# Kernel tuning notes

Hardware: AMD Instinct MI355X
Metric: run time of the kernel (lower is better)

The kernel has to match this reference:

```python
import jax, jax.numpy as jnp
import numpy as np

B, S, D, H = 2, 2048, 2048, 16
DK = D // H
THETA = 10000.0


def setup_inputs() -> dict:
    key = jax.random.key(0)
    ks = jax.random.split(key, 5)
    scale = 0.02
    return {
        "x": jax.random.normal(ks[0], (B, S, D), dtype=jnp.float32),
        "W_Q": jax.random.normal(ks[1], (D, D), dtype=jnp.float32) * scale,
        "W_K": jax.random.normal(ks[2], (D, D), dtype=jnp.float32) * scale,
        "W_V": jax.random.normal(ks[3], (D, D), dtype=jnp.float32) * scale,
        "W_O": jax.random.normal(ks[4], (D, D), dtype=jnp.float32) * scale,
        "token_positions": jnp.arange(S, dtype=jnp.int32),
    }


def _rope(x, pos):
    # x: [B, S, H, DK]; pos: [S]. Interleaved-pair rotation (cs336 RoPE).
    half = DK // 2
    inv_freq = THETA ** (-(jnp.arange(half, dtype=jnp.float32) / half))  # [half]
    ang = pos.astype(jnp.float32)[:, None] * inv_freq[None, :]           # [S, half]
    cos = jnp.cos(ang)[None, :, None, :]                                 # [1,S,1,half]
    sin = jnp.sin(ang)[None, :, None, :]
    x1, x2 = x[..., ::2], x[..., 1::2]
    r1 = x1 * cos - x2 * sin
    r2 = x1 * sin + x2 * cos
    return jnp.stack([r1, r2], axis=-1).reshape(x.shape)


def reference(x, W_Q, W_K, W_V, W_O, token_positions):
    # QKV projections (Linear with no bias: y = x @ W^T)
    Q = (x @ W_Q.T).reshape(B, S, H, DK)
    K = (x @ W_K.T).reshape(B, S, H, DK)
    V = (x @ W_V.T).reshape(B, S, H, DK)
    Q = _rope(Q, token_positions)
    K = _rope(K, token_positions)
    scores = jnp.einsum("bqhd,bkhd->bhqk", Q, K) / jnp.sqrt(jnp.float32(DK))
    causal = jnp.tril(jnp.ones((S, S), dtype=bool))  # True = attend
    scores = jnp.where(causal[None, None], scores, -jnp.inf)
    attn = jax.nn.softmax(scores, axis=-1)
    out = jnp.einsum("bhqk,bkhd->bqhd", attn, V).reshape(B, S, D)
    return out @ W_O.T
```

## Files before the change

### kernel.cpp

```cpp
#include <hip/hip_runtime.h>
#include <hip/hip_bf16.h>
#include <cstdint>
#include <cstddef>

#define B_ 2
#define S_ 2048
#define D_ 2048
#define H_ 16
#define DK_ 128
#define M_ (B_*S_)

typedef __attribute__((ext_vector_type(8))) __bf16 bf16x8;
typedef __attribute__((ext_vector_type(4))) float f32x4;
typedef __attribute__((ext_vector_type(16))) float f32x16;

__device__ __forceinline__ unsigned short f2bf(float f) {
  union { float f; unsigned int u; } v; v.f = f;
  unsigned int r = (v.u + 0x7fffu + ((v.u >> 16) & 1u)) >> 16;
  return (unsigned short)r;
}
__device__ __forceinline__ float bf2f(unsigned short b) {
  union { unsigned int u; float f; } v; v.u = ((unsigned int)b) << 16;
  return v.f;
}

__device__ __forceinline__ void gld16(const void* g, void* l) {
  __builtin_amdgcn_global_load_lds(
      (const __attribute__((address_space(1))) unsigned int*)g,
      (__attribute__((address_space(3))) unsigned int*)l, 16, 0, 0);
}

__global__ void cvt_all(const float* __restrict__ x,  const float* __restrict__ Wq,
                        const float* __restrict__ Wk, const float* __restrict__ Wv,
                        const float* __restrict__ Wo, unsigned short* __restrict__ dst) {
  size_t i = ((size_t)blockIdx.x * blockDim.x + threadIdx.x) * 4;
  const float* src;
  size_t off;
  if (i < ((size_t)M_ * D_)) {
    src = x; off = i;
  } else {
    size_t j = i - (size_t)M_ * D_;
    int w = (int)(j >> 22);
    off = j & ((1u << 22) - 1);
    src = (w == 0) ? Wq : (w == 1) ? Wk : (w == 2) ? Wv : Wo;
  }
  float4 v = *(const float4*)(src + off);
  dst[i+0] = f2bf(v.x); dst[i+1] = f2bf(v.y);
  dst[i+2] = f2bf(v.z); dst[i+3] = f2bf(v.w);
}

__global__ __launch_bounds__(512, 2) void gemm_qkv(const unsigned short* __restrict__ A,
                                                   const unsigned short* __restrict__ W0,
                                                   const unsigned short* __restrict__ W1,
                                                   const unsigned short* __restrict__ W2,
                                                   unsigned short* __restrict__ C0,
                                                   unsigned short* __restrict__ C1,
                                                   unsigned short* __restrict__ C2,
                                                   int M, int N, int K) {
  __shared__ unsigned short sA[2][2][256 * 32];
  __shared__ unsigned short sB[2][2][256 * 32];
  const int id   = blockIdx.x;
  const int tid  = threadIdx.x;
  const int lane = tid & 63;
  const int wid  = tid >> 6;
  const int l16 = lane & 15, quad = lane >> 4;
  const int col16 = quad ^ ((lane >> 1) & 3);
  const int qk_log = (lane & 3) ^ ((lane >> 3) & 3);
  const int srow = lane >> 2;
  const int NT = K >> 6;

  if (id < 256) {
    const int z = id >> 7, r = id & 127;
    const unsigned short* Bt = z ? W1 : W0;
    unsigned short* Cout = z ? C1 : C0;
    const int bm = (r >> 3) * 256, bn = (r & 7) * 256;
    const int wm = wid >> 2, wn = wid & 3;

    f32x4 acc[8][4];
    #pragma unroll
    for (int i = 0; i < 8; ++i)
      #pragma unroll
      for (int j = 0; j < 4; ++j)
        acc[i][j] = (f32x4){0.f, 0.f, 0.f, 0.f};

    auto stage = [&](const unsigned short* __restrict__ g, int rowbase,
                     unsigned short* l, int t, int kh) {
      const unsigned short* src = g + (size_t)rowbase * K + t * 64 + kh * 32 + qk_log * 8;
      #pragma unroll
      for (int p = 0; p < 2; ++p) {
        const int i = wid * 2 + p;
        gld16(src + (size_t)(i * 16 + srow) * K, l + i * 512);
      }
    };

    stage(A,  bm, &sA[0][0][0], 0, 0);
    stage(Bt, bn, &sB[0][0][0], 0, 0);
    stage(A,  bm, &sA[0][1][0], 0, 1);
    stage(Bt, bn, &sB[0][1][0], 0, 1);
    stage(A,  bm, &sA[1][0][0], 1, 0);
    stage(Bt, bn, &sB[1][0][0], 1, 0);
    asm volatile("s_waitcnt vmcnt(4)" ::: "memory");
    __builtin_amdgcn_s_barrier();

    for (int t = 0; t < NT; ++t) {
      const int buf = t & 1;
      bf16x8 bfrag[4];
      #pragma unroll
      for (int ph = 0; ph < 4; ++ph) {
        const int ks = ph >> 1;
        const int mh = ph & 1;
        bf16x8 afrag[4];
        const unsigned short* aP = &sA[buf][ks][0] +
            (size_t)((wm * 128 + mh * 64 + l16) * 4 + col16) * 8;
        #pragma unroll
        for (int mf = 0; mf < 4; ++mf)
          afrag[mf] = *(const bf16x8*)(aP + mf * 512);
        if (mh == 0) {
          const unsigned short* bP = &sB[buf][ks][0] +
              (size_t)((wn * 64 + l16) * 4 + col16) * 8;
          #pragma unroll
          for (int nf = 0; nf < 4; ++nf)
            bfrag[nf] = *(const bf16x8*)(bP + nf * 512);
        }
        if (ph == 0)      { if (t + 1 < NT) stage(A,  bm, &sA[buf ^ 1][1][0], t + 1, 1); }
        else if (ph == 1) { if (t + 1 < NT) stage(Bt, bn, &sB[buf ^ 1][1][0], t + 1, 1); }
        else if (ph == 2) { if (t + 2 < NT) stage(A,  bm, &sA[buf][0][0],     t + 2, 0); }
        else              { if (t + 2 < NT) stage(Bt, bn, &sB[buf][0][0],     t + 2, 0); }

        __builtin_amdgcn_s_barrier();
        asm volatile("s_waitcnt lgkmcnt(0)" ::: "memory");
        __builtin_amdgcn_s_setprio(1);
        #pragma unroll
        for (int nf = 0; nf < 4; ++nf)
          #pragma unroll
          for (int mf = 0; mf < 4; ++mf)
            acc[mh * 4 + mf][nf] = __builtin_amdgcn_mfma_f32_16x16x32_bf16(
                afrag[mf], bfrag[nf], acc[mh * 4 + mf][nf], 0, 0, 0);
        __builtin_amdgcn_s_setprio(0);
        if (ph == 3) {
          if (t + 2 < NT) asm volatile("s_waitcnt vmcnt(4)" ::: "memory");
          else            asm volatile("s_waitcnt vmcnt(0)" ::: "memory");
        }
        __builtin_amdgcn_s_barrier();
      }
    }

    #pragma unroll
    for (int mf = 0; mf < 8; ++mf) {
      const int row = bm + wm * 128 + mf * 16 + quad * 4;
      #pragma unroll
      for (int nf = 0; nf < 4; ++nf) {
        const int col = bn + wn * 64 + nf * 16 + l16;
        #pragma unroll
        for (int rr = 0; rr < 4; ++rr)
          Cout[(size_t)(row + rr) * N + col] = f2bf(acc[mf][nf][rr]);
      }
    }
  } else {
    const int r = id - 256;
    const unsigned short* Bt = W2;
    unsigned short* Cout = C2;
    const int bm = (r >> 3) * 128, bn = (r & 7) * 256;
    const int wm = wid >> 2, wn = wid & 3;

    f32x4 acc[4][4];
    #pragma unroll
    for (int i = 0; i < 4; ++i)
      #pragma unroll
      for (int j = 0; j < 4; ++j)
        acc[i][j] = (f32x4){0.f, 0.f, 0.f, 0.f};

    auto stageB = [&](unsigned short* l, int t, int kh) {
      const unsigned short* src = Bt + (size_t)bn * K + t * 64 + kh * 32 + qk_log * 8;
      #pragma unroll
      for (int p = 0; p < 2; ++p) {
        const int i = wid * 2 + p;
        gld16(src + (size_t)(i * 16 + srow) * K, l + i * 512);
      }
    };
    auto stageA = [&](unsigned short* l, int t, int kh) {
      const unsigned short* src = A + (size_t)bm * K + t * 64 + kh * 32 + qk_log * 8;
      gld16(src + (size_t)(wid * 16 + srow) * K, l + wid * 512);
    };

    stageA(&sA[0][0][0], 0, 0); stageB(&sB[0][0][0], 0, 0);
    stageA(&sA[0][1][0], 0, 1); stageB(&sB[0][1][0], 0, 1);
    stageA(&sA[1][0][0], 1, 0); stageB(&sB[1][0][0], 1, 0);
    asm volatile("s_waitcnt vmcnt(3)" ::: "memory");
    __builtin_amdgcn_s_barrier();

    for (int t = 0; t < NT; ++t) {
      const int buf = t & 1;
      #pragma unroll
      for (int ph = 0; ph < 2; ++ph) {
        bf16x8 afrag[4], bfrag[4];
        const unsigned short* aP = &sA[buf][ph][0] +
            (size_t)((wm * 64 + l16) * 4 + col16) * 8;
        #pragma unroll
        for (int mf = 0; mf < 4; ++mf)
          afrag[mf] = *(const bf16x8*)(aP + mf * 512);
        const unsigned short* bP = &sB[buf][ph][0] +
            (size_t)((wn * 64 + l16) * 4 + col16) * 8;
        #pragma unroll
        for (int nf = 0; nf < 4; ++nf)
          bfrag[nf] = *(const bf16x8*)(bP + nf * 512);

        if (ph == 0) { if (t + 1 < NT) { stageA(&sA[buf ^ 1][1][0], t + 1, 1);
                                         stageB(&sB[buf ^ 1][1][0], t + 1, 1); } }
        else         { if (t + 2 < NT) { stageA(&sA[buf][0][0], t + 2, 0);
                                         stageB(&sB[buf][0][0], t + 2, 0); } }

        __builtin_amdgcn_s_barrier();
        asm volatile("s_waitcnt lgkmcnt(0)" ::: "memory");
        __builtin_amdgcn_s_setprio(1);
        #pragma unroll
        for (int nf = 0; nf < 4; ++nf)
          #pragma unroll
          for (int mf = 0; mf < 4; ++mf)
            acc[mf][nf] = __builtin_amdgcn_mfma_f32_16x16x32_bf16(
                afrag[mf], bfrag[nf], acc[mf][nf], 0, 0, 0);
        __builtin_amdgcn_s_setprio(0);
        if (ph == 1) {
          if (t + 2 < NT) asm volatile("s_waitcnt vmcnt(3)" ::: "memory");
          else            asm volatile("s_waitcnt vmcnt(0)" ::: "memory");
        }
        __builtin_amdgcn_s_barrier();
      }
    }

    #pragma unroll
    for (int mf = 0; mf < 4; ++mf) {
      const int row = bm + wm * 64 + mf * 16 + quad * 4;
      #pragma unroll
      for (int nf = 0; nf < 4; ++nf) {
        const int col = bn + wn * 64 + nf * 16 + l16;
        #pragma unroll
        for (int rr = 0; rr < 4; ++rr)
          Cout[(size_t)(row + rr) * N + col] = f2bf(acc[mf][nf][rr]);
      }
    }
  }
}

__global__ __launch_bounds__(512, 2) void gemm_out(const unsigned short* __restrict__ A,
                                                   const unsigned short* __restrict__ Bt,
                                                   float* __restrict__ C,
                                                   int M, int N, int K) {
  __shared__ unsigned short sA[2][2][256 * 32];
  __shared__ unsigned short sB[2][2][128 * 32];
  const int id   = blockIdx.x;
  const int tid  = threadIdx.x;
  const int lane = tid & 63;
  const int wid  = tid >> 6;
  const int l16 = lane & 15, quad = lane >> 4;
  const int col16 = quad ^ ((lane >> 1) & 3);
  const int qk_log = (lane & 3) ^ ((lane >> 3) & 3);
  const int srow = lane >> 2;
  const int NT = K >> 6;
  const int bm = (id >> 4) * 256, bn = (id & 15) * 128;
  const int wm = wid >> 1, wn = wid & 1;

  f32x4 acc[4][4];
  #pragma unroll
  for (int i = 0; i < 4; ++i)
    #pragma unroll
    for (int j = 0; j < 4; ++j)
      acc[i][j] = (f32x4){0.f, 0.f, 0.f, 0.f};

  auto stageA = [&](unsigned short* l, int t, int kh) {
    const unsigned short* src = A + (size_t)bm * K + t * 64 + kh * 32 + qk_log * 8;
    #pragma unroll
    for (int p = 0; p < 2; ++p) {
      const int i = wid * 2 + p;
      gld16(src + (size_t)(i * 16 + srow) * K, l + i * 512);
    }
  };
  auto stageB = [&](unsigned short* l, int t, int kh) {
    const unsigned short* src = Bt + (size_t)bn * K + t * 64 + kh * 32 + qk_log * 8;
    gld16(src + (size_t)(wid * 16 + srow) * K, l + wid * 512);
  };

  stageA(&sA[0][0][0], 0, 0); stageB(&sB[0][0][0], 0, 0);
  stageA(&sA[0][1][0], 0, 1); stageB(&sB[0][1][0], 0, 1);
  stageA(&sA[1][0][0], 1, 0); stageB(&sB[1][0][0], 1, 0);
  asm volatile("s_waitcnt vmcnt(3)" ::: "memory");
  __builtin_amdgcn_s_barrier();

  for (int t = 0; t < NT; ++t) {
    const int buf = t & 1;
    #pragma unroll
    for (int ph = 0; ph < 2; ++ph) {
      bf16x8 afrag[4], bfrag[4];
      const unsigned short* aP = &sA[buf][ph][0] +
          (size_t)((wm * 64 + l16) * 4 + col16) * 8;
      #pragma unroll
      for (int mf = 0; mf < 4; ++mf)
        afrag[mf] = *(const bf16x8*)(aP + mf * 512);
      const unsigned short* bP = &sB[buf][ph][0] +
          (size_t)((wn * 64 + l16) * 4 + col16) * 8;
      #pragma unroll
      for (int nf = 0; nf < 4; ++nf)
        bfrag[nf] = *(const bf16x8*)(bP + nf * 512);

      if (ph == 0) { if (t + 1 < NT) { stageA(&sA[buf ^ 1][1][0], t + 1, 1);
                                       stageB(&sB[buf ^ 1][1][0], t + 1, 1); } }
      else         { if (t + 2 < NT) { stageA(&sA[buf][0][0], t + 2, 0);
                                       stageB(&sB[buf][0][0], t + 2, 0); } }

      __builtin_amdgcn_s_barrier();
      asm volatile("s_waitcnt lgkmcnt(0)" ::: "memory");
      __builtin_amdgcn_s_setprio(1);
      #pragma unroll
      for (int nf = 0; nf < 4; ++nf)
        #pragma unroll
        for (int mf = 0; mf < 4; ++mf)
          acc[mf][nf] = __builtin_amdgcn_mfma_f32_16x16x32_bf16(
              afrag[mf], bfrag[nf], acc[mf][nf], 0, 0, 0);
      __builtin_amdgcn_s_setprio(0);
      if (ph == 1) {
        if (t + 2 < NT) asm volatile("s_waitcnt vmcnt(3)" ::: "memory");
        else            asm volatile("s_waitcnt vmcnt(0)" ::: "memory");
      }
      __builtin_amdgcn_s_barrier();
    }
  }

  #pragma unroll
  for (int mf = 0; mf < 4; ++mf) {
    const int row = bm + wm * 64 + mf * 16 + quad * 4;
    #pragma unroll
    for (int nf = 0; nf < 4; ++nf) {
      const int col = bn + wn * 64 + nf * 16 + l16;
      #pragma unroll
      for (int rr = 0; rr < 4; ++rr)
        C[(size_t)(row + rr) * N + col] = acc[mf][nf][rr];
    }
  }
}

__global__ void rope_kernel(unsigned short* __restrict__ Q, unsigned short* __restrict__ K,
                            const int* __restrict__ pos) {
  int idx = blockIdx.x * blockDim.x + threadIdx.x;
  int i = idx & 63;
  int h = (idx >> 6) & (H_ - 1);
  int s = (idx >> 10) & (S_ - 1);
  int b = idx >> 21;
  float p = (float)pos[s];
  float inv = __expf(-(float)i * (9.210340371976184f / 64.0f));
  float ang = p * inv;
  float sn, cs;
  __sincosf(ang, &sn, &cs);
  size_t base = (((size_t)b * S_ + s) * D_) + (size_t)h * DK_ + 2 * i;
  unsigned int q2 = *(const unsigned int*)(Q + base);
  float x1 = bf2f((unsigned short)(q2 & 0xffffu)), x2 = bf2f((unsigned short)(q2 >> 16));
  unsigned int lo = f2bf(x1 * cs - x2 * sn), hi = f2bf(x1 * sn + x2 * cs);
  *(unsigned int*)(Q + base) = lo | (hi << 16);
  unsigned int k2 = *(const unsigned int*)(K + base);
  x1 = bf2f((unsigned short)(k2 & 0xffffu)); x2 = bf2f((unsigned short)(k2 >> 16));
  lo = f2bf(x1 * cs - x2 * sn); hi = f2bf(x1 * sn + x2 * cs);
  *(unsigned int*)(K + base) = lo | (hi << 16);
}

__global__ __launch_bounds__(256) void transpose_bf16(const unsigned short* __restrict__ src,
                                                      unsigned short* __restrict__ dst) {
  __shared__ unsigned short sT[64 * 64];
  const int b = blockIdx.y;
  const int tx = blockIdx.x & 31, ty = blockIdx.x >> 5;
  const size_t base = (size_t)b * 2048 * 2048;
  const int m0 = ty * 64, c0 = tx * 64;
  const int tid = threadIdx.x;
  #pragma unroll
  for (int c = 0; c < 2; ++c) {
    int idx = tid + c * 256;
    int row = idx >> 3;
    int chk = idx & 7;
    uint4 v = *(const uint4*)(src + base + (size_t)(m0 + row) * 2048 + c0 + chk * 8);
    *(uint4*)(sT + row * 64 + ((chk ^ (row & 7)) * 8)) = v;
  }
  __syncthreads();
  #pragma unroll
  for (int c = 0; c < 2; ++c) {
    int idx = tid + c * 256;
    int orow = idx >> 3;
    int ocol = (idx & 7) * 8;
    unsigned short tmp[8];
    #pragma unroll
    for (int j = 0; j < 8; ++j) {
      int lr = ocol + j;
      int lc = orow;
      tmp[j] = sT[lr * 64 + (((lc >> 3) ^ (lr & 7)) * 8) + (lc & 7)];
    }
    *(uint4*)(dst + base + (size_t)(c0 + orow) * 2048 + m0 + ocol) = *(const uint4*)tmp;
  }
}

__global__ __launch_bounds__(256, 2) void flash_attn(const unsigned short* __restrict__ Q,
                                                     const unsigned short* __restrict__ K,
                                                     const unsigned short* __restrict__ VT,
                                                     unsigned short* __restrict__ O) {
  __shared__ unsigned short sK[2][64 * 128];
  __shared__ unsigned short sVT[2][128 * 64];
  __shared__ unsigned short sP[4][32 * 64];

  const int tid = threadIdx.x, lane = tid & 63, wid = tid >> 6;
  const int half = lane >> 5, l32 = lane & 31;
  const int qi = 15 - (blockIdx.x & 15);
  const int bh = blockIdx.x >> 4;
  const int h = bh & (H_ - 1), b = bh >> 4;
  const int qw = qi * 128 + wid * 32;
  const size_t qkbase = ((size_t)b * S_) * D_ + (size_t)h * DK_;
  const unsigned short* Qg = Q + qkbase;
  const unsigned short* Kg = K + qkbase;
  const unsigned short* VTg = VT + (size_t)bh * DK_ * S_;
  unsigned short* Og = O + qkbase;
  unsigned short* sPw = sP[wid];

  const int kKeySub = lane >> 4;
  const int kPhys   = lane & 15;
  const int vFeatSub = lane >> 3;
  const int vPhys    = lane & 7;

  bf16x8 qf[8];
  #pragma unroll
  for (int ks = 0; ks < 8; ++ks)
    qf[ks] = *(const bf16x8*)(Qg + (size_t)(qw + l32) * D_ + ks * 16 + half * 8);

  union { unsigned short u[8]; bf16x8 v; } onesu;
  #pragma unroll
  for (int j2 = 0; j2 < 8; ++j2) onesu.u[j2] = 0x3F80;
  const bf16x8 ones = onesu.v;

  f32x16 Oacc[4];
  #pragma unroll
  for (int ft = 0; ft < 4; ++ft)
    #pragma unroll
    for (int r = 0; r < 16; ++r) Oacc[ft][r] = 0.f;
  f32x16 l_acc;
  #pragma unroll
  for (int r = 0; r < 16; ++r) l_acc[r] = 0.f;
  const float scale = 0.08838834764831845f;

  const int nkb = 2 * (qi + 1);

  auto stage = [&](int kb) {
    const int k0 = kb * 64;
    unsigned short* bK = sK[kb & 1];
    unsigned short* bV = sVT[kb & 1];
    #pragma unroll
    for (int p = 0; p < 4; ++p) {
      int issue = wid * 4 + p;
      int key = issue * 4 + kKeySub;
      int logiK = (kPhys & 8) | ((kPhys ^ key) & 7);
      gld16(Kg + (size_t)(k0 + key) * D_ + logiK * 8, bK + issue * 512);
      int feat = issue * 8 + vFeatSub;
      int logiV = vPhys ^ (feat & 7);
      gld16(VTg + (size_t)feat * S_ + k0 + logiV * 8, bV + issue * 512);
    }
  };

  stage(0);

  for (int kb = 0; kb < nkb; ++kb) {
    __syncthreads();
    if (kb + 1 < nkb) stage(kb + 1);

    const int k0 = kb * 64;
    if (k0 > qw + 31) continue;

    const unsigned short* bK = sK[kb & 1];
    const unsigned short* bV = sVT[kb & 1];

    f32x16 sc[2];
    #pragma unroll
    for (int t = 0; t < 2; ++t)
      #pragma unroll
      for (int r = 0; r < 16; ++r) sc[t][r] = 0.f;
    __builtin_amdgcn_s_setprio(1);
    #pragma unroll
    for (int ks = 0; ks < 8; ++ks) {
      const int logi = ks * 2 + half;
      #pragma unroll
      for (int t = 0; t < 2; ++t) {
        const int key = t * 32 + l32;
        const int phys = (logi & 8) | ((logi ^ key) & 7);
        bf16x8 kf = *(const bf16x8*)(bK + key * 128 + phys * 8);
        sc[t] = __builtin_amdgcn_mfma_f32_32x32x16_bf16(qf[ks], kf, sc[t], 0, 0, 0);
      }
    }
    __builtin_amdgcn_s_setprio(0);

    const bool diag = (k0 + 63 > qw);
    #pragma unroll
    for (int t = 0; t < 2; ++t) {
      const int col = t * 32 + l32;
      const int keyg = k0 + col;
      #pragma unroll
      for (int r = 0; r < 16; ++r) {
        const int rl = (r & 3) + 8 * (r >> 2) + 4 * half;
        float v = sc[t][r] * scale;
        if (diag && (keyg > qw + rl)) v = -1e30f;
        sPw[rl * 64 + (((col >> 3) ^ (rl & 7)) * 8) + (col & 7)] = f2bf(__expf(v));
      }
    }

    __builtin_amdgcn_s_setprio(1);
    #pragma unroll
    for (int ksp = 0; ksp < 4; ++ksp) {
      const int logi = ksp * 2 + half;
      bf16x8 pf = *(const bf16x8*)(sPw + l32 * 64 + ((logi ^ (l32 & 7)) * 8));
      l_acc = __builtin_amdgcn_mfma_f32_32x32x16_bf16(pf, ones, l_acc, 0, 0, 0);
      #pragma unroll
      for (int ft = 0; ft < 4; ++ft) {
        const int feat = ft * 32 + l32;
        const int phys = logi ^ (feat & 7);
        bf16x8 vf = *(const bf16x8*)(bV + feat * 64 + phys * 8);
        Oacc[ft] = __builtin_amdgcn_mfma_f32_32x32x16_bf16(pf, vf, Oacc[ft], 0, 0, 0);
      }
    }
    __builtin_amdgcn_s_setprio(0);
  }

  #pragma unroll
  for (int ft = 0; ft < 4; ++ft) {
    const int feat = ft * 32 + l32;
    #pragma unroll
    for (int r = 0; r < 16; ++r) {
      const int rl = (r & 3) + 8 * (r >> 2) + 4 * half;
      Og[(size_t)(qw + rl) * D_ + feat] = f2bf(Oacc[ft][r] / l_acc[r]);
    }
  }
}

extern "C" void kernel_launch(void* const* d_in, const int* in_sizes, int n_in,
                              void* d_out, int out_size, void* d_ws, size_t ws_size,
                              hipStream_t stream) {
  const float* x  = (const float*)d_in[0];
  const float* Wq = (const float*)d_in[1];
  const float* Wk = (const float*)d_in[2];
  const float* Wv = (const float*)d_in[3];
  const float* Wo = (const float*)d_in[4];
  const int*  pos = (const int*)d_in[5];
  float* out = (float*)d_out;

  char* ws = (char*)d_ws;
  size_t off = 0;
  auto alloc = [&](size_t bytes) { void* p = ws + off; off += (bytes + 255) & ~255ULL; return p; };
  const size_t nx = (size_t)M_ * D_;
  const size_t nw = (size_t)D_ * D_;
  unsigned short* xb  = (unsigned short*)alloc(nx * 2);
  unsigned short* wqb = (unsigned short*)alloc(nw * 2);
  unsigned short* wkb = (unsigned short*)alloc(nw * 2);
  unsigned short* wvb = (unsigned short*)alloc(nw * 2);
  unsigned short* wob = (unsigned short*)alloc(nw * 2);
  unsigned short* Qb  = (unsigned short*)alloc(nx * 2);
  unsigned short* Kb  = (unsigned short*)alloc(nx * 2);
  unsigned short* Vb  = (unsigned short*)alloc(nx * 2);
  unsigned short* AOb = xb;
  unsigned short* VTb = wqb;

  hipLaunchKernelGGL(cvt_all, dim3((nx + 4 * nw) / 1024), dim3(256), 0, stream,
                     x, Wq, Wk, Wv, Wo, xb);

  hipLaunchKernelGGL(gemm_qkv, dim3(512), dim3(512), 0, stream,
                     xb, wqb, wkb, wvb, Qb, Kb, Vb, M_, D_, D_);

  hipLaunchKernelGGL(rope_kernel, dim3((B_ * S_ * H_ * 64) / 256), dim3(256), 0, stream, Qb, Kb, pos);

  hipLaunchKernelGGL(transpose_bf16, dim3(1024, 2), dim3(256), 0, stream, Vb, VTb);

  hipLaunchKernelGGL(flash_attn, dim3(B_ * H_ * (S_ / 128)), dim3(256), 0, stream, Qb, Kb, VTb, AOb);

  hipLaunchKernelGGL(gemm_out, dim3((M_ / 256) * (D_ / 128)), dim3(512), 0, stream,
                     AOb, wob, out, M_, D_, D_);
}
```

Measured before the change: 411.4 us.

## Fuse RoPE and V transpose into the QKV GEMM epilogue

Applies RoPE to Q and K inside the QKV GEMM epilogue, using lane shuffles to pair interleaved elements, and writes V directly in transposed [b,h,dk,s] layout. This removes the separate rope and transpose kernels along with their extra global memory round trips and launches. The cost is sincos work in the GEMM epilogue and strided 8-byte stores for V^T, which coalesce worse than row-major stores.

```diff
diff --git a/kernel.cpp b/kernel.cpp
--- a/kernel.cpp
+++ b/kernel.cpp
@@ -55,7 +55,8 @@
                                                    const unsigned short* __restrict__ W2,
                                                    unsigned short* __restrict__ C0,
                                                    unsigned short* __restrict__ C1,
-                                                   unsigned short* __restrict__ C2,
+                                                   unsigned short* __restrict__ CVT,
+                                                   const int* __restrict__ pos,
                                                    int M, int N, int K) {
   __shared__ unsigned short sA[2][2][256 * 32];
   __shared__ unsigned short sB[2][2][256 * 32];
@@ -145,6 +146,30 @@
       }
     }
 
+    float invf[4];
+    #pragma unroll
+    for (int nf = 0; nf < 4; ++nf) {
+      const int i = (((wn & 1) * 64) + nf * 16 + l16) >> 1;
+      invf[nf] = __expf(-(float)i * (9.210340371976184f / 64.0f));
+    }
+    const float ssgn = (lane & 1) ? 1.0f : -1.0f;
+    #pragma unroll
+    for (int mf = 0; mf < 8; ++mf) {
+      const int row = bm + wm * 128 + mf * 16 + quad * 4;
+      #pragma unroll
+      for (int rr = 0; rr < 4; ++rr) {
+        const float p = (float)pos[(row + rr) & (S_ - 1)];
+        #pragma unroll
+        for (int nf = 0; nf < 4; ++nf) {
+          float sn, cs;
+          __sincosf(p * invf[nf], &sn, &cs);
+          const float v = acc[mf][nf][rr];
+          const float xo = __shfl_xor(v, 1);
+          acc[mf][nf][rr] = v * cs + xo * (sn * ssgn);
+        }
+      }
+    }
+
     #pragma unroll
     for (int mf = 0; mf < 8; ++mf) {
       const int row = bm + wm * 128 + mf * 16 + quad * 4;
@@ -159,7 +184,6 @@
   } else {
     const int r = id - 256;
     const unsigned short* Bt = W2;
-    unsigned short* Cout = C2;
     const int bm = (r >> 3) * 128, bn = (r & 7) * 256;
     const int wm = wid >> 2, wn = wid & 3;
 
@@ -231,12 +255,16 @@
     #pragma unroll
     for (int mf = 0; mf < 4; ++mf) {
       const int row = bm + wm * 64 + mf * 16 + quad * 4;
+      const int s = row & (S_ - 1), bidx = row >> 11;
       #pragma unroll
       for (int nf = 0; nf < 4; ++nf) {
         const int col = bn + wn * 64 + nf * 16 + l16;
-        #pragma unroll
-        for (int rr = 0; rr < 4; ++rr)
-          Cout[(size_t)(row + rr) * N + col] = f2bf(acc[mf][nf][rr]);
+        const int bh = bidx * 16 + (col >> 7);
+        const int dk = col & 127;
+        unsigned short tmp[4];
+        #pragma unroll
+        for (int rr = 0; rr < 4; ++rr) tmp[rr] = f2bf(acc[mf][nf][rr]);
+        *(uint2*)(CVT + ((size_t)bh * DK_ + dk) * S_ + s) = *(const uint2*)tmp;
       }
     }
   }
@@ -338,62 +366,6 @@
   }
 }
 
-__global__ void rope_kernel(unsigned short* __restrict__ Q, unsigned short* __restrict__ K,
-                            const int* __restrict__ pos) {
-  int idx = blockIdx.x * blockDim.x + threadIdx.x;
-  int i = idx & 63;
-  int h = (idx >> 6) & (H_ - 1);
-  int s = (idx >> 10) & (S_ - 1);
-  int b = idx >> 21;
-  float p = (float)pos[s];
-  float inv = __expf(-(float)i * (9.210340371976184f / 64.0f));
-  float ang = p * inv;
-  float sn, cs;
-  __sincosf(ang, &sn, &cs);
-  size_t base = (((size_t)b * S_ + s) * D_) + (size_t)h * DK_ + 2 * i;
-  unsigned int q2 = *(const unsigned int*)(Q + base);
-  float x1 = bf2f((unsigned short)(q2 & 0xffffu)), x2 = bf2f((unsigned short)(q2 >> 16));
-  unsigned int lo = f2bf(x1 * cs - x2 * sn), hi = f2bf(x1 * sn + x2 * cs);
-  *(unsigned int*)(Q + base) = lo | (hi << 16);
-  unsigned int k2 = *(const unsigned int*)(K + base);
-  x1 = bf2f((unsigned short)(k2 & 0xffffu)); x2 = bf2f((unsigned short)(k2 >> 16));
-  lo = f2bf(x1 * cs - x2 * sn); hi = f2bf(x1 * sn + x2 * cs);
-  *(unsigned int*)(K + base) = lo | (hi << 16);
-}
-
-__global__ __launch_bounds__(256) void transpose_bf16(const unsigned short* __restrict__ src,
-                                                      unsigned short* __restrict__ dst) {
-  __shared__ unsigned short sT[64 * 64];
-  const int b = blockIdx.y;
-  const int tx = blockIdx.x & 31, ty = blockIdx.x >> 5;
-  const size_t base = (size_t)b * 2048 * 2048;
-  const int m0 = ty * 64, c0 = tx * 64;
-  const int tid = threadIdx.x;
-  #pragma unroll
-  for (int c = 0; c < 2; ++c) {
-    int idx = tid + c * 256;
-    int row = idx >> 3;
-    int chk = idx & 7;
-    uint4 v = *(const uint4*)(src + base + (size_t)(m0 + row) * 2048 + c0 + chk * 8);
-    *(uint4*)(sT + row * 64 + ((chk ^ (row & 7)) * 8)) = v;
-  }
-  __syncthreads();
-  #pragma unroll
-  for (int c = 0; c < 2; ++c) {
-    int idx = tid + c * 256;
-    int orow = idx >> 3;
-    int ocol = (idx & 7) * 8;
-    unsigned short tmp[8];
-    #pragma unroll
-    for (int j = 0; j < 8; ++j) {
-      int lr = ocol + j;
-      int lc = orow;
-      tmp[j] = sT[lr * 64 + (((lc >> 3) ^ (lr & 7)) * 8) + (lc & 7)];
-    }
-    *(uint4*)(dst + base + (size_t)(c0 + orow) * 2048 + m0 + ocol) = *(const uint4*)tmp;
-  }
-}
-
 __global__ __launch_bounds__(256, 2) void flash_attn(const unsigned short* __restrict__ Q,
                                                      const unsigned short* __restrict__ K,
                                                      const unsigned short* __restrict__ VT,
@@ -554,19 +526,14 @@
   unsigned short* wob = (unsigned short*)alloc(nw * 2);
   unsigned short* Qb  = (unsigned short*)alloc(nx * 2);
   unsigned short* Kb  = (unsigned short*)alloc(nx * 2);
-  unsigned short* Vb  = (unsigned short*)alloc(nx * 2);
+  unsigned short* VTb = (unsigned short*)alloc(nx * 2);
   unsigned short* AOb = xb;
-  unsigned short* VTb = wqb;
 
   hipLaunchKernelGGL(cvt_all, dim3((nx + 4 * nw) / 1024), dim3(256), 0, stream,
                      x, Wq, Wk, Wv, Wo, xb);
 
   hipLaunchKernelGGL(gemm_qkv, dim3(512), dim3(512), 0, stream,
-                     xb, wqb, wkb, wvb, Qb, Kb, Vb, M_, D_, D_);
-
-  hipLaunchKernelGGL(rope_kernel, dim3((B_ * S_ * H_ * 64) / 256), dim3(256), 0, stream, Qb, Kb, pos);
-
-  hipLaunchKernelGGL(transpose_bf16, dim3(1024, 2), dim3(256), 0, stream, Vb, VTb);
+                     xb, wqb, wkb, wvb, Qb, Kb, VTb, pos, M_, D_, D_);
 
   hipLaunchKernelGGL(flash_attn, dim3(B_ * H_ * (S_ / 128)), dim3(256), 0, stream, Qb, Kb, VTb, AOb);
 
```

After: 392.0 us. -4.7%, faster.
